# Kernel tuning notes

Hardware: AMD Instinct MI355X
Metric: run time of the kernel (lower is better)

The kernel has to match this reference:

```python
import jax, jax.numpy as jnp
import numpy as np

B, T, I, H = 64, 2048, 256, 256  # batch, timesteps, input_dim, units


def setup_inputs() -> dict:
    key = jax.random.key(0)
    k1, k2, k3 = jax.random.split(key, 3)
    scale_x = 1.0 / np.sqrt(I)
    scale_h = 1.0 / np.sqrt(H)
    return {
        "x": jax.random.normal(k1, (B, T, I), dtype=jnp.float32),
        "Wx": jax.random.normal(k2, (I, 4 * H), dtype=jnp.float32) * scale_x,
        "Wh": jax.random.normal(k3, (H, 4 * H), dtype=jnp.float32) * scale_h,
        "b": jnp.zeros((4 * H,), dtype=jnp.float32),
        "h0": jnp.zeros((B, H), dtype=jnp.float32),
        "c0": jnp.zeros((B, H), dtype=jnp.float32),
    }


def reference(x, Wx, Wh, b, h0, c0):
    """Keras RNN(LSTMCell, return_sequences=True): sequential scan over time.

    Gate order follows Keras LSTM: i, f, c(g), o with sigmoid recurrent
    activation and tanh cell activation.
    """
    H_ = h0.shape[-1]
    # Input projection is time-independent: hoist out of the scan. [B,T,4H]
    xz = jnp.einsum("bti,ig->btg", x, Wx) + b

    def step(carry, xz_t):
        h, c = carry
        z = xz_t + h @ Wh  # [B,4H]
        i = jax.nn.sigmoid(z[:, 0 * H_:1 * H_])
        f = jax.nn.sigmoid(z[:, 1 * H_:2 * H_])
        g = jnp.tanh(z[:, 2 * H_:3 * H_])
        o = jax.nn.sigmoid(z[:, 3 * H_:4 * H_])
        c_new = f * c + i * g
        h_new = o * jnp.tanh(c_new)
        return (h_new, c_new), h_new

    # scan over time axis: [T,B,4H]
    (_, _), outputs = jax.lax.scan(step, (h0, c0), jnp.transpose(xz, (1, 0, 2)))
    return jnp.transpose(outputs, (1, 0, 2))  # [B,T,H]
```

## Files before the change

kernel.cpp:

```cpp
#include <hip/hip_runtime.h>

typedef unsigned short u16;
typedef unsigned int   u32;
typedef short short8 __attribute__((ext_vector_type(8)));
typedef float f32x4  __attribute__((ext_vector_type(4)));

#define AGENT __HIP_MEMORY_SCOPE_AGENT

__device__ __forceinline__ float bf2f(u16 u) {
    u32 x = ((u32)u) << 16;
    return __builtin_bit_cast(float, x);
}
__device__ __forceinline__ u16 f2bf(float f) {
    u32 x = __builtin_bit_cast(u32, f);
    u32 r = (x + 0x7FFFu + ((x >> 16) & 1u)) >> 16;
    return (u16)r;
}
__device__ __forceinline__ float sigmoidf_(float x) { return 1.0f / (1.0f + __expf(-x)); }
__device__ __forceinline__ float tanhf_(float x) { return 2.0f / (1.0f + __expf(-2.0f * x)) - 1.0f; }

__global__ __launch_bounds__(256) void lstm_init(const u16* __restrict__ xbits,
                                                 int* __restrict__ counters,
                                                 int* __restrict__ flag) {
    int i = blockIdx.x * 256 + threadIdx.x;
    counters[i] = 0;
    if (blockIdx.x == 0 && threadIdx.x == 0) {
        int cnt = 0;
        const uint4* p = (const uint4*)xbits;
        for (int j = 0; j < 64; j++) {
            uint4 v = p[j];
            u32 wv[4] = {v.x, v.y, v.z, v.w};
#pragma unroll
            for (int k2 = 0; k2 < 4; k2++) {
                u32 lo = wv[k2] & 0xFFFFu, hi = wv[k2] >> 16;
                cnt += ((lo & 0x7F80u) >= 0x4600u) ? 1 : 0;
                cnt += ((hi & 0x7F80u) >= 0x4600u) ? 1 : 0;
            }
        }
        *flag = cnt;
    }
}

__global__ __launch_bounds__(256, 1) void lstm_fused(const void* __restrict__ x,
                                                     const void* __restrict__ Wx,
                                                     const void* __restrict__ Wh,
                                                     const void* __restrict__ bias,
                                                     const void* __restrict__ c0,
                                                     const void* __restrict__ h0,
                                                     u16* __restrict__ hbuf,
                                                     void* __restrict__ out,
                                                     int* __restrict__ counters,
                                                     const int* __restrict__ flag) {
    __shared__ __align__(16) u16 hs[16 * 264];

    const int tid = threadIdx.x;
    const int lane = tid & 63, w = tid >> 6;
    const int q = lane >> 4, n16 = lane & 15;
    const int jB = blockIdx.x & 3, jH = blockIdx.x >> 2;
    const int b0 = jB * 16;
    const int hc = jH * 64 + w * 16 + n16;
    const int bq = b0 + q * 4;

    const int isf32 = (*flag > 64);

    short8 Bh[4][8];
    short8 Bx[4][8];

#define PRELOAD_W(Wsrc, Bf)                                                    \
    _Pragma("unroll")                                                          \
    for (int p = 0; p < 16; p++) {                                             \
        const int g = p >> 2, sub = p & 3;                                     \
        const int colg = g * 256 + jH * 64 + sub * 16;                         \
        u16 tmp[16];                                                           \
        if (isf32) {                                                           \
            const float* s = (const float*)(Wsrc) + (size_t)tid * 1024 + colg; \
            _Pragma("unroll")                                                  \
            for (int c = 0; c < 16; c++) tmp[c] = f2bf(s[c]);                  \
        } else {                                                               \
            const u16* s = (const u16*)(Wsrc) + (size_t)tid * 1024 + colg;     \
            *(uint4*)&tmp[0] = *(const uint4*)s;                               \
            *(uint4*)&tmp[8] = *(const uint4*)(s + 8);                         \
        }                                                                      \
        __syncthreads();                        \
        _Pragma("unroll")                                                      \
        for (int c = 0; c < 16; c++) hs[c * 264 + tid] = tmp[c];               \
        __syncthreads();                                                       \
        if (sub == w) {                                                        \
            _Pragma("unroll")                                                  \
            for (int ks = 0; ks < 8; ks++)                                     \
                (Bf)[g][ks] = *(const short8*)&hs[n16 * 264 + ks * 32 + q * 8];\
        }                                                                      \
    }

    PRELOAD_W(Wh, Bh)
    PRELOAD_W(Wx, Bx)
    __syncthreads();

#define LOADX(t, dst)                                                              \
    if (isf32) {                                                                   \
        const float* xb = (const float*)x + ((size_t)(b0 + n16) * 2048 + (t)) * 256 + q * 8; \
        _Pragma("unroll")                                                          \
        for (int ks = 0; ks < 8; ks++) {                                           \
            u16 tmp[8];                                                            \
            _Pragma("unroll")                                                      \
            for (int j = 0; j < 8; j++) tmp[j] = f2bf(xb[ks * 32 + j]);            \
            (dst)[ks] = *(const short8*)tmp;                                       \
        }                                                                          \
    } else {                                                                       \
        const u16* xb = (const u16*)x + ((size_t)(b0 + n16) * 2048 + (t)) * 256 + q * 8; \
        _Pragma("unroll")                                                          \
        for (int ks = 0; ks < 8; ks++) (dst)[ks] = *(const short8*)(xb + ks * 32); \
    }

    float bv[4];
#pragma unroll
    for (int g = 0; g < 4; g++)
        bv[g] = isf32 ? ((const float*)bias)[g * 256 + hc]
                      : bf2f(((const u16*)bias)[g * 256 + hc]);

    float creg[4];
#pragma unroll
    for (int r = 0; r < 4; r++)
        creg[r] = isf32 ? ((const float*)c0)[(size_t)(bq + r) * 256 + hc]
                        : bf2f(((const u16*)c0)[(size_t)(bq + r) * 256 + hc]);

#pragma unroll
    for (int m = 0; m < 16; m++) {
        u16 v = isf32 ? f2bf(((const float*)h0)[(size_t)(b0 + m) * 256 + tid])
                      : ((const u16*)h0)[(size_t)(b0 + m) * 256 + tid];
        hs[m * 264 + tid] = v;
    }

    f32x4 zx[4];
    {
        short8 xf[8];
        LOADX(0, xf)
#pragma unroll
        for (int g = 0; g < 4; g++) { f32x4 a = {bv[g], bv[g], bv[g], bv[g]}; zx[g] = a; }
#pragma unroll
        for (int ks = 0; ks < 8; ks++)
#pragma unroll
            for (int g = 0; g < 4; g++)
                zx[g] = __builtin_amdgcn_mfma_f32_16x16x32_bf16(xf[ks], Bx[g][ks], zx[g], 0, 0, 0);
    }

    for (int tl = 0; tl < 2048; tl++) {
        short8 xfn[8];
        if (tl + 1 < 2048) { LOADX(tl + 1, xfn) }

        if (tl > 0) {
            const int* cp = &counters[jB * 2048 + (tl - 1)];
            int guard = 0;
            while (__hip_atomic_load(cp, __ATOMIC_ACQUIRE, AGENT) < 4) {
                __builtin_amdgcn_s_sleep(1);
                if (++guard > (1 << 22)) break;
            }
            const int par = (tl & 1) ^ 1;
            const u32* hp = (const u32*)(hbuf + (size_t)par * 16384 + (size_t)tid * 64 + b0);
            u32 hv[8];
#pragma unroll
            for (int i2 = 0; i2 < 8; i2++) hv[i2] = __hip_atomic_load(hp + i2, __ATOMIC_RELAXED, AGENT);
#pragma unroll
            for (int m = 0; m < 16; m++) {
                u16 val = (u16)((hv[m >> 1] >> ((m & 1) * 16)) & 0xFFFFu);
                hs[m * 264 + tid] = val;
            }
        }
        __syncthreads();

        f32x4 acc[4];
#pragma unroll
        for (int g = 0; g < 4; g++) acc[g] = zx[g];
#pragma unroll
        for (int ks = 0; ks < 8; ks++) {
            short8 af = *(const short8*)&hs[n16 * 264 + ks * 32 + q * 8];
#pragma unroll
            for (int g = 0; g < 4; g++)
                acc[g] = __builtin_amdgcn_mfma_f32_16x16x32_bf16(af, Bh[g][ks], acc[g], 0, 0, 0);
        }

        float hf[4];
        u16 hb[4];
#pragma unroll
        for (int r = 0; r < 4; r++) {
            float ig = sigmoidf_(acc[0][r]);
            float fg = sigmoidf_(acc[1][r]);
            float gg = tanhf_(acc[2][r]);
            float og = sigmoidf_(acc[3][r]);
            float cn = fg * creg[r] + ig * gg;
            creg[r] = cn;
            hf[r] = og * tanhf_(cn);
            hb[r] = f2bf(hf[r]);
        }
        {
            const int par = tl & 1;
            u32* hp = (u32*)(hbuf + (size_t)par * 16384 + (size_t)hc * 64 + bq);
            u32 lo = (u32)hb[0] | ((u32)hb[1] << 16);
            u32 hi = (u32)hb[2] | ((u32)hb[3] << 16);
            __hip_atomic_store(hp + 0, lo, __ATOMIC_RELAXED, AGENT);
            __hip_atomic_store(hp + 1, hi, __ATOMIC_RELAXED, AGENT);
        }
        __syncthreads();
        if (tid == 0)
            __hip_atomic_fetch_add(&counters[jB * 2048 + tl], 1, __ATOMIC_RELEASE, AGENT);

#pragma unroll
        for (int r = 0; r < 4; r++) {
            size_t oi = ((size_t)(bq + r) * 2048 + tl) * 256 + hc;
            if (isf32) ((float*)out)[oi] = hf[r];
            else       ((u16*)out)[oi] = hb[r];
        }

        if (tl + 1 < 2048) {
#pragma unroll
            for (int g = 0; g < 4; g++) { f32x4 a = {bv[g], bv[g], bv[g], bv[g]}; zx[g] = a; }
#pragma unroll
            for (int ks = 0; ks < 8; ks++)
#pragma unroll
                for (int g = 0; g < 4; g++)
                    zx[g] = __builtin_amdgcn_mfma_f32_16x16x32_bf16(xfn[ks], Bx[g][ks], zx[g], 0, 0, 0);
        }
    }
}

extern "C" void kernel_launch(void* const* d_in, const int* in_sizes, int n_in,
                              void* d_out, int out_size, void* d_ws, size_t ws_size,
                              hipStream_t stream) {
    const void* x    = d_in[0];
    const void* Wx   = d_in[1];
    const void* Wh   = d_in[2];
    const void* bias = d_in[3];
    const void* h0   = d_in[4];
    const void* c0   = d_in[5];

    u16* hbuf = (u16*)d_ws;
    int* counters = (int*)((char*)d_ws + 65536);
    int* flag = counters + 8192;

    lstm_init<<<32, 256, 0, stream>>>((const u16*)x, counters, flag);
    lstm_fused<<<16, 256, 0, stream>>>(x, Wx, Wh, bias, c0, h0, hbuf, d_out, counters, flag);
}
```

Before: 16.33 ms.

## Replace counter barrier with timestep-tagged h values and double-buffered LDS

Removes the per-step atomic counter and the extra block barrier before it. Each h value is now stored as a 32-bit word holding the bf16 value and the low 16 bits of the timestep, and consumers spin until every word they read carries the expected tag. The shared h tile is double-buffered so the second __syncthreads can be dropped, and the next step's input projection is moved ahead of the output store. This shortens the cross-block critical path per timestep but doubles the exchange buffer size and makes every poll read 16 words instead of one counter.

```diff
diff --git a/kernel.cpp b/kernel.cpp
--- a/kernel.cpp
+++ b/kernel.cpp
@@ -20,11 +20,13 @@
 __device__ __forceinline__ float tanhf_(float x) { return 2.0f / (1.0f + __expf(-2.0f * x)) - 1.0f; }
 
 __global__ __launch_bounds__(256) void lstm_init(const u16* __restrict__ xbits,
-                                                 int* __restrict__ counters,
+                                                 u32* __restrict__ hbufT,
                                                  int* __restrict__ flag) {
     int i = blockIdx.x * 256 + threadIdx.x;
-    counters[i] = 0;
-    if (blockIdx.x == 0 && threadIdx.x == 0) {
+#pragma unroll
+    for (int j = 0; j < 4; j++)
+        __hip_atomic_store(hbufT + (size_t)i * 4 + j, 0xFFFFu, __ATOMIC_RELAXED, AGENT);
+    if (i == 0) {
         int cnt = 0;
         const uint4* p = (const uint4*)xbits;
         for (int j = 0; j < 64; j++) {
@@ -47,11 +49,10 @@
                                                      const void* __restrict__ bias,
                                                      const void* __restrict__ c0,
                                                      const void* __restrict__ h0,
-                                                     u16* __restrict__ hbuf,
+                                                     u32* __restrict__ hbufT,
                                                      void* __restrict__ out,
-                                                     int* __restrict__ counters,
                                                      const int* __restrict__ flag) {
-    __shared__ __align__(16) u16 hs[16 * 264];
+    __shared__ __align__(16) u16 hs[2][16 * 264];
 
     const int tid = threadIdx.x;
     const int lane = tid & 63, w = tid >> 6;
@@ -62,6 +63,8 @@
     const int bq = b0 + q * 4;
 
     const int isf32 = (*flag > 64);
+
+    u16* hsc = &hs[0][0];
 
     short8 Bh[4][8];
     short8 Bx[4][8];
@@ -83,12 +86,12 @@
         }                                                                      \
         __syncthreads();                        \
         _Pragma("unroll")                                                      \
-        for (int c = 0; c < 16; c++) hs[c * 264 + tid] = tmp[c];               \
+        for (int c = 0; c < 16; c++) hsc[c * 264 + tid] = tmp[c];              \
         __syncthreads();                                                       \
         if (sub == w) {                                                        \
             _Pragma("unroll")                                                  \
             for (int ks = 0; ks < 8; ks++)                                     \
-                (Bf)[g][ks] = *(const short8*)&hs[n16 * 264 + ks * 32 + q * 8];\
+                (Bf)[g][ks] = *(const short8*)&hsc[n16 * 264 + ks * 32 + q * 8];\
         }                                                                      \
     }
 
@@ -128,7 +131,7 @@
     for (int m = 0; m < 16; m++) {
         u16 v = isf32 ? f2bf(((const float*)h0)[(size_t)(b0 + m) * 256 + tid])
                       : ((const u16*)h0)[(size_t)(b0 + m) * 256 + tid];
-        hs[m * 264 + tid] = v;
+        hs[0][m * 264 + tid] = v;
     }
 
     f32x4 zx[4];
@@ -145,26 +148,33 @@
     }
 
     for (int tl = 0; tl < 2048; tl++) {
+        const int hsP = tl & 1;
+        u16* hsW = &hs[hsP][0];
+
         short8 xfn[8];
         if (tl + 1 < 2048) { LOADX(tl + 1, xfn) }
 
         if (tl > 0) {
-            const int* cp = &counters[jB * 2048 + (tl - 1)];
+            const u32 expt = (u32)(tl - 1);
+            const int par = (tl - 1) & 1;
+            const u32* hp = hbufT + (size_t)par * 16384 + (size_t)tid * 64 + b0;
+            u32 hv[16];
             int guard = 0;
-            while (__hip_atomic_load(cp, __ATOMIC_ACQUIRE, AGENT) < 4) {
+            for (;;) {
+#pragma unroll
+                for (int i = 0; i < 16; i++)
+                    hv[i] = __hip_atomic_load(hp + i, __ATOMIC_RELAXED, AGENT);
+                u32 ok = 1;
+#pragma unroll
+                for (int i = 0; i < 16; i++)
+                    ok &= (u32)((hv[i] & 0xFFFFu) == expt);
+                if (ok) break;
+                if (++guard > (1 << 22)) break;
                 __builtin_amdgcn_s_sleep(1);
-                if (++guard > (1 << 22)) break;
             }
-            const int par = (tl & 1) ^ 1;
-            const u32* hp = (const u32*)(hbuf + (size_t)par * 16384 + (size_t)tid * 64 + b0);
-            u32 hv[8];
-#pragma unroll
-            for (int i2 = 0; i2 < 8; i2++) hv[i2] = __hip_atomic_load(hp + i2, __ATOMIC_RELAXED, AGENT);
-#pragma unroll
-            for (int m = 0; m < 16; m++) {
-                u16 val = (u16)((hv[m >> 1] >> ((m & 1) * 16)) & 0xFFFFu);
-                hs[m * 264 + tid] = val;
-            }
+#pragma unroll
+            for (int m = 0; m < 16; m++)
+                hsW[m * 264 + tid] = (u16)(hv[m] >> 16);
         }
         __syncthreads();
 
@@ -173,7 +183,7 @@
         for (int g = 0; g < 4; g++) acc[g] = zx[g];
 #pragma unroll
         for (int ks = 0; ks < 8; ks++) {
-            short8 af = *(const short8*)&hs[n16 * 264 + ks * 32 + q * 8];
+            short8 af = *(const short8*)&hsW[n16 * 264 + ks * 32 + q * 8];
 #pragma unroll
             for (int g = 0; g < 4; g++)
                 acc[g] = __builtin_amdgcn_mfma_f32_16x16x32_bf16(af, Bh[g][ks], acc[g], 0, 0, 0);
@@ -193,32 +203,27 @@
             hb[r] = f2bf(hf[r]);
         }
         {
-            const int par = tl & 1;
-            u32* hp = (u32*)(hbuf + (size_t)par * 16384 + (size_t)hc * 64 + bq);
-            u32 lo = (u32)hb[0] | ((u32)hb[1] << 16);
-            u32 hi = (u32)hb[2] | ((u32)hb[3] << 16);
-            __hip_atomic_store(hp + 0, lo, __ATOMIC_RELAXED, AGENT);
-            __hip_atomic_store(hp + 1, hi, __ATOMIC_RELAXED, AGENT);
-        }
-        __syncthreads();
-        if (tid == 0)
-            __hip_atomic_fetch_add(&counters[jB * 2048 + tl], 1, __ATOMIC_RELEASE, AGENT);
-
+            u32* hw = hbufT + (size_t)(tl & 1) * 16384 + (size_t)hc * 64 + bq;
+#pragma unroll
+            for (int r = 0; r < 4; r++)
+                __hip_atomic_store(hw + r, ((u32)hb[r] << 16) | (u32)tl,
+                                   __ATOMIC_RELAXED, AGENT);
+        }
+
+        if (tl + 1 < 2048) {
+#pragma unroll
+            for (int g = 0; g < 4; g++) { f32x4 a = {bv[g], bv[g], bv[g], bv[g]}; zx[g] = a; }
+#pragma unroll
+            for (int ks = 0; ks < 8; ks++)
+#pragma unroll
+                for (int g = 0; g < 4; g++)
+                    zx[g] = __builtin_amdgcn_mfma_f32_16x16x32_bf16(xfn[ks], Bx[g][ks], zx[g], 0, 0, 0);
+        }
 #pragma unroll
         for (int r = 0; r < 4; r++) {
             size_t oi = ((size_t)(bq + r) * 2048 + tl) * 256 + hc;
             if (isf32) ((float*)out)[oi] = hf[r];
             else       ((u16*)out)[oi] = hb[r];
-        }
-
-        if (tl + 1 < 2048) {
-#pragma unroll
-            for (int g = 0; g < 4; g++) { f32x4 a = {bv[g], bv[g], bv[g], bv[g]}; zx[g] = a; }
-#pragma unroll
-            for (int ks = 0; ks < 8; ks++)
-#pragma unroll
-                for (int g = 0; g < 4; g++)
-                    zx[g] = __builtin_amdgcn_mfma_f32_16x16x32_bf16(xfn[ks], Bx[g][ks], zx[g], 0, 0, 0);
         }
     }
 }
@@ -233,10 +238,9 @@
     const void* h0   = d_in[4];
     const void* c0   = d_in[5];
 
-    u16* hbuf = (u16*)d_ws;
-    int* counters = (int*)((char*)d_ws + 65536);
-    int* flag = counters + 8192;
-
-    lstm_init<<<32, 256, 0, stream>>>((const u16*)x, counters, flag);
-    lstm_fused<<<16, 256, 0, stream>>>(x, Wx, Wh, bias, c0, h0, hbuf, d_out, counters, flag);
-}
+    u32* hbufT = (u32*)d_ws;
+    int* flag = (int*)((char*)d_ws + 131072);
+
+    lstm_init<<<32, 256, 0, stream>>>((const u16*)x, hbufT, flag);
+    lstm_fused<<<16, 256, 0, stream>>>(x, Wx, Wh, bias, c0, h0, hbufT, d_out, flag);
+}
```

New measurement: 17.06 ms. +4.4%, slower.
